# Kernel tuning notes

Hardware: AMD Instinct MI355X
Metric: run time of the kernel (lower is better)

The kernel has to match this reference:

```python
import jax, jax.numpy as jnp
from jax import lax
import numpy as np

V = 50000          # num_word; embedding table has V+1 rows
D = 512            # embedding_dim / d_model
H = 8              # nhead
FF = 2048          # dim_feedforward (hidden_dim)
L = 32             # num_label (incl START/STOP)
START, STOP = L - 2, L - 1
S = 2048           # sentence length
NEG = -10000.0


def setup_inputs() -> dict:
    k = jax.random.split(jax.random.key(0), 10)
    def rn(key, shape, s=0.02):
        return jax.random.normal(key, shape, jnp.float32) * s
    transitions = jax.random.normal(k[8], (L, L), jnp.float32)
    transitions = transitions.at[START, :].set(NEG).at[:, STOP].set(NEG)
    return {
        "sentence": jax.random.randint(k[0], (S,), 0, V + 1),
        "embed": rn(k[1], (V + 1, D), 1.0),
        "Wqkv": rn(k[2], (3 * D, D)), "bqkv": jnp.zeros((3 * D,), jnp.float32),
        "Wo": rn(k[3], (D, D)), "bo": jnp.zeros((D,), jnp.float32),
        "ln1_g": jnp.ones((D,), jnp.float32), "ln1_b": jnp.zeros((D,), jnp.float32),
        "W1": rn(k[4], (FF, D)), "b1": jnp.zeros((FF,), jnp.float32),
        "W2": rn(k[5], (D, FF)), "b2": jnp.zeros((D,), jnp.float32),
        "ln2_g": jnp.ones((D,), jnp.float32), "ln2_b": jnp.zeros((D,), jnp.float32),
        "Wt": rn(k[6], (L, D)), "bt": jnp.zeros((L,), jnp.float32),
        "transitions": transitions,
    }


def _ln(x, g, b):
    m = jnp.mean(x, -1, keepdims=True)
    v = jnp.var(x, -1, keepdims=True)
    return (x - m) * lax.rsqrt(v + 1e-5) * g + b


def _transformer_feats(sentence, embed, Wqkv, bqkv, Wo, bo, ln1_g, ln1_b,
                       W1, b1, W2, b2, ln2_g, ln2_b, Wt, bt):
    x = embed[sentence]                                   # [S, D]
    qkv = x @ Wqkv.T + bqkv                               # [S, 3D]
    q, k, v = jnp.split(qkv, 3, axis=-1)
    to_heads = lambda t: t.reshape(S, H, D // H).transpose(1, 0, 2)  # [H, S, dh]
    q, k, v = to_heads(q), to_heads(k), to_heads(v)
    att = jax.nn.softmax(jnp.einsum('hsd,htd->hst', q, k) / np.float32(np.sqrt(D // H)), axis=-1)
    o = jnp.einsum('hst,htd->hsd', att, v).transpose(1, 0, 2).reshape(S, D)
    # post-norm TransformerEncoderLayer (eval mode: dropout off), relu FFN
    x = _ln(x + o @ Wo.T + bo, ln1_g, ln1_b)
    ff = jax.nn.relu(x @ W1.T + b1) @ W2.T + b2
    x = _ln(x + ff, ln2_g, ln2_b)
    return x @ Wt.T + bt                                  # [S, L] emission scores


def _viterbi(feats, transitions):
    init = jnp.full((L,), NEG, jnp.float32).at[START].set(0.0)
    def step(prev, emit):
        scores = prev[None, :] + transitions              # [next_tag, prev_tag]
        bp = jnp.argmax(scores, axis=1)                   # best prev tag per next tag
        return jnp.max(scores, axis=1) + emit, bp
    last, bps = lax.scan(step, init, feats)               # bps: [S, L]
    terminal = last + transitions[STOP]
    best = jnp.argmax(terminal)
    def back(tag, bp):
        return bp[tag], tag
    _, path = lax.scan(back, best, bps, reverse=True)     # path[t] = best tag at step t
    return terminal[best], path


def reference(sentence, embed, Wqkv, bqkv, Wo, bo, ln1_g, ln1_b,
              W1, b1, W2, b2, ln2_g, ln2_b, Wt, bt, transitions):
    feats = _transformer_feats(sentence, embed, Wqkv, bqkv, Wo, bo, ln1_g, ln1_b,
                               W1, b1, W2, b2, ln2_g, ln2_b, Wt, bt)
    score, path = _viterbi(feats, transitions)
    return score, path
```

## Files before the change

### kernel.cpp

```cpp
#include <hip/hip_runtime.h>
#include <cstddef>

#define S_LEN 2048
#define D_MODEL 512
#define NHEAD 8
#define DH 64
#define FF_DIM 2048
#define L_TAGS 32
#define START_TAG 30
#define STOP_TAG 31
#define NEGV (-10000.0f)
#define QSCALE 0.18033688f

typedef unsigned int uint2v __attribute__((ext_vector_type(2)));
typedef __attribute__((ext_vector_type(8))) short short8v;
typedef __attribute__((ext_vector_type(4))) float f32x4;

union U8 { uint4 u; short8v s; };

__device__ __forceinline__ unsigned short f2bf(float f) {
  unsigned u = __float_as_uint(f);
  u += 0x7fff + ((u >> 16) & 1);
  return (unsigned short)(u >> 16);
}
__device__ __forceinline__ unsigned cvtpk(float lo, float hi) {
  unsigned r;
  asm("v_cvt_pk_bf16_f32 %0, %1, %2" : "=v"(r) : "v"(lo), "v"(hi));
  return r;
}

__global__ __launch_bounds__(256) void k_f2h4(const float* __restrict__ s0, short* __restrict__ d0,
                                              const float* __restrict__ s1, short* __restrict__ d1,
                                              const float* __restrict__ s2, short* __restrict__ d2,
                                              const float* __restrict__ s3, short* __restrict__ d3) {
  const int b = blockIdx.x;
  const float* src; short* dst; int i;
  if (b < 384)       { src = s0; dst = d0; i = b * 256 + threadIdx.x; }
  else if (b < 512)  { src = s1; dst = d1; i = (b - 384) * 256 + threadIdx.x; }
  else if (b < 1024) { src = s2; dst = d2; i = (b - 512) * 256 + threadIdx.x; }
  else               { src = s3; dst = d3; i = (b - 1024) * 256 + threadIdx.x; }
  f32x4 a = *(const f32x4*)(src + (size_t)i * 8);
  f32x4 c = *(const f32x4*)(src + (size_t)i * 8 + 4);
  U8 t;
  t.u.x = cvtpk(a[0], a[1]); t.u.y = cvtpk(a[2], a[3]);
  t.u.z = cvtpk(c[0], c[1]); t.u.w = cvtpk(c[2], c[3]);
  *(short8v*)(dst + (size_t)i * 8) = t.s;
}

__global__ __launch_bounds__(256, 2) void k_gemm_qkv(const int* __restrict__ sent,
                                                     const float* __restrict__ embed,
                                                     const short* __restrict__ B,
                                                     const float* __restrict__ bias,
                                                     short* __restrict__ C,
                                                     int N, int K) {
  __shared__ __align__(16) short As[2][128 * 64];
  __shared__ __align__(16) short Bs[2][128 * 64];
  const int tid = threadIdx.x;
  const int nwg = gridDim.x * gridDim.y;
  int lin = blockIdx.x + gridDim.x * blockIdx.y;
  int wk = (lin & 7) * (nwg >> 3) + (lin >> 3);
  const int bxs = wk % gridDim.x, bys = wk / gridDim.x;
  const int bm = bys * 128, bn = bxs * 128;
  const int w = tid >> 6, lane = tid & 63;
  const int wr = w >> 1, wc = w & 1;
  const int fr = lane & 15, kg = lane >> 4;
  const int srow = tid >> 1, sc0 = (tid & 1) * 4;
  const int swz = srow & 7;
  const float* gA = embed + (size_t)sent[bm + srow] * K + sc0 * 8;
  const short* gB = B + (size_t)(bn + srow) * K + sc0 * 8;
  f32x4 ra[8];
  short8v rb[4];
  f32x4 acc[4][4] = {};

  auto loadg = [&](int k0) {
#pragma unroll
    for (int c = 0; c < 4; ++c) {
      ra[2 * c] = *(const f32x4*)(gA + k0 + c * 8);
      ra[2 * c + 1] = *(const f32x4*)(gA + k0 + c * 8 + 4);
      rb[c] = *(const short8v*)(gB + k0 + c * 8);
    }
  };
  auto storeb = [&](int b) {
    short* dA = &As[b][srow * 64];
    short* dB = &Bs[b][srow * 64];
#pragma unroll
    for (int c = 0; c < 4; ++c) {
      U8 ta;
      ta.u.x = cvtpk(ra[2 * c][0], ra[2 * c][1]);
      ta.u.y = cvtpk(ra[2 * c][2], ra[2 * c][3]);
      ta.u.z = cvtpk(ra[2 * c + 1][0], ra[2 * c + 1][1]);
      ta.u.w = cvtpk(ra[2 * c + 1][2], ra[2 * c + 1][3]);
      *(short8v*)(dA + (((sc0 + c) ^ swz) << 3)) = ta.s;
      *(short8v*)(dB + (((sc0 + c) ^ swz) << 3)) = rb[c];
    }
  };

  loadg(0);
  storeb(0);
  __syncthreads();
  int cur = 0;
  const int fswz = fr & 7;
  for (int k0 = 0; k0 < K; k0 += 64) {
    const bool more = (k0 + 64) < K;
    if (more) loadg(k0 + 64);
    const short* rA = &As[cur][(wr * 64 + fr) * 64];
    const short* rB = &Bs[cur][(wc * 64 + fr) * 64];
#pragma unroll
    for (int ks = 0; ks < 2; ++ks) {
      const int co = ((ks * 4 + kg) ^ fswz) << 3;
      short8v af[4], bf[4];
#pragma unroll
      for (int rt = 0; rt < 4; ++rt) af[rt] = *(const short8v*)(rA + rt * 16 * 64 + co);
#pragma unroll
      for (int ct = 0; ct < 4; ++ct) bf[ct] = *(const short8v*)(rB + ct * 16 * 64 + co);
#pragma unroll
      for (int rt = 0; rt < 4; ++rt)
#pragma unroll
        for (int ct = 0; ct < 4; ++ct)
          acc[rt][ct] = __builtin_amdgcn_mfma_f32_16x16x32_bf16(af[rt], bf[ct], acc[rt][ct], 0, 0, 0);
    }
    if (more) storeb(cur ^ 1);
    __syncthreads();
    cur ^= 1;
  }
#pragma unroll
  for (int rt = 0; rt < 4; ++rt) {
#pragma unroll
    for (int ct = 0; ct < 4; ++ct) {
      f32x4 v = acc[rt][ct];
      const int row0 = bm + wr * 64 + rt * 16 + kg * 4;
      const int col = bn + wc * 64 + ct * 16 + fr;
      const float bs = bias[col];
#pragma unroll
      for (int j = 0; j < 4; ++j)
        C[(size_t)(row0 + j) * N + col] = (short)f2bf(v[j] + bs);
    }
  }
}

template <int RT, bool RELU, bool OBF>
__global__ __launch_bounds__(256, 2) void k_gemm_bf(const short* __restrict__ A,
                                                    const short* __restrict__ B,
                                                    const float* __restrict__ bias,
                                                    void* __restrict__ Cp,
                                                    int M, int N, int K) {
  constexpr int BM = RT * 32;
  constexpr int CH = (BM * 8) / 256;
  __shared__ __align__(16) short As[2][BM * 64];
  __shared__ __align__(16) short Bs[2][BM * 64];
  const int tid = threadIdx.x;
  const int nwg = gridDim.x * gridDim.y;
  int lin = blockIdx.x + gridDim.x * blockIdx.y;
  int wk = (lin & 7) * (nwg >> 3) + (lin >> 3);
  const int bxs = wk % gridDim.x, bys = wk / gridDim.x;
  const int bm = bys * BM, bn = bxs * BM;
  const int w = tid >> 6, lane = tid & 63;
  const int wr = w >> 1, wc = w & 1;
  const int fr = lane & 15, kg = lane >> 4;
  const int srow = (RT == 4) ? (tid >> 1) : (tid >> 2);
  const int sc0 = (RT == 4) ? ((tid & 1) * 4) : ((tid & 3) * 2);
  const int swz = srow & 7;
  const short* gA = A + (size_t)(bm + srow) * K + sc0 * 8;
  const short* gB = B + (size_t)(bn + srow) * K + sc0 * 8;
  short8v ra[CH], rb[CH];
  f32x4 acc[RT][RT] = {};

  auto loadg = [&](int k0) {
#pragma unroll
    for (int c = 0; c < CH; ++c) {
      ra[c] = *(const short8v*)(gA + k0 + c * 8);
      rb[c] = *(const short8v*)(gB + k0 + c * 8);
    }
  };
  auto storeb = [&](int b) {
    short* dA = &As[b][srow * 64];
    short* dB = &Bs[b][srow * 64];
#pragma unroll
    for (int c = 0; c < CH; ++c) {
      *(short8v*)(dA + (((sc0 + c) ^ swz) << 3)) = ra[c];
      *(short8v*)(dB + (((sc0 + c) ^ swz) << 3)) = rb[c];
    }
  };

  loadg(0);
  storeb(0);
  __syncthreads();
  int cur = 0;
  const int fswz = fr & 7;
  for (int k0 = 0; k0 < K; k0 += 64) {
    const bool more = (k0 + 64) < K;
    if (more) loadg(k0 + 64);
    const short* rA = &As[cur][(wr * (RT * 16) + fr) * 64];
    const short* rB = &Bs[cur][(wc * (RT * 16) + fr) * 64];
#pragma unroll
    for (int ks = 0; ks < 2; ++ks) {
      const int co = ((ks * 4 + kg) ^ fswz) << 3;
      short8v af[RT], bf[RT];
#pragma unroll
      for (int rt = 0; rt < RT; ++rt) af[rt] = *(const short8v*)(rA + rt * 16 * 64 + co);
#pragma unroll
      for (int ct = 0; ct < RT; ++ct) bf[ct] = *(const short8v*)(rB + ct * 16 * 64 + co);
#pragma unroll
      for (int rt = 0; rt < RT; ++rt)
#pragma unroll
        for (int ct = 0; ct < RT; ++ct)
          acc[rt][ct] = __builtin_amdgcn_mfma_f32_16x16x32_bf16(af[rt], bf[ct], acc[rt][ct], 0, 0, 0);
    }
    if (more) storeb(cur ^ 1);
    __syncthreads();
    cur ^= 1;
  }
#pragma unroll
  for (int rt = 0; rt < RT; ++rt) {
#pragma unroll
    for (int ct = 0; ct < RT; ++ct) {
      f32x4 v = acc[rt][ct];
      const int row0 = bm + wr * (RT * 16) + rt * 16 + kg * 4;
      const int col = bn + wc * (RT * 16) + ct * 16 + fr;
      const float bs = bias[col];
#pragma unroll
      for (int j = 0; j < 4; ++j) {
        float o = v[j] + bs;
        if (RELU) o = fmaxf(o, 0.f);
        if (OBF)
          ((short*)Cp)[(size_t)(row0 + j) * N + col] = (short)f2bf(o);
        else
          ((float*)Cp)[(size_t)(row0 + j) * N + col] = o;
      }
    }
  }
}

__global__ __launch_bounds__(256) void k_attn(const short* __restrict__ qkv,
                                              short* __restrict__ ob) {
  __shared__ __align__(16) short Ks[2][64 * 64];
  __shared__ __align__(16) short Vt[2][64 * 72];
  __shared__ __align__(16) short Pl[4][16 * 72];
  const int tid = threadIdx.x;
  const int b = blockIdx.x;
  const int h = b & 7;
  const int bq = (b >> 3) * 64;
  const int wq = tid >> 6, lane = tid & 63;
  const int fr = lane & 15, kg = lane >> 4;
  auto scale8 = [](short8v q) -> short8v {
    unsigned wv[4];
#pragma unroll
    for (int i = 0; i < 4; ++i) {
      float lo = __uint_as_float(((unsigned)(unsigned short)q[2 * i]) << 16) * QSCALE;
      float hi = __uint_as_float(((unsigned)(unsigned short)q[2 * i + 1]) << 16) * QSCALE;
      wv[i] = cvtpk(lo, hi);
    }
    U8 t;
    t.u.x = wv[0]; t.u.y = wv[1]; t.u.z = wv[2]; t.u.w = wv[3];
    return t.s;
  };
  short8v qf[2];
  {
    const short* qsrc = qkv + (size_t)(bq + wq * 16 + fr) * 1536 + h * DH;
    qf[0] = scale8(*(const short8v*)(qsrc + kg * 8));
    qf[1] = scale8(*(const short8v*)(qsrc + 32 + kg * 8));
  }
  float m[4], l[4];
  f32x4 oac[4] = {};
#pragma unroll
  for (int j = 0; j < 4; ++j) { m[j] = -1e30f; l[j] = 0.f; }

  const int srow = tid >> 2, sc0 = (tid & 3) * 2;
  const int kpair = tid & 31, dgrp = tid >> 5;
  short8v kr0, kr1, va, vb;
  auto loadt = [&](int kt) {
    const short* kbase = qkv + (size_t)(kt * 64 + srow) * 1536 + 512 + h * DH;
    kr0 = *(const short8v*)(kbase + sc0 * 8);
    kr1 = *(const short8v*)(kbase + sc0 * 8 + 8);
    const short* vbase = qkv + (size_t)(kt * 64 + 2 * kpair) * 1536 + 1024 + h * DH + dgrp * 8;
    va = *(const short8v*)(vbase);
    vb = *(const short8v*)(vbase + 1536);
  };
  auto storet = [&](int cu) {
    short* dk = &Ks[cu][srow * 64];
    *(short8v*)(dk + ((sc0 ^ (srow & 7)) << 3)) = kr0;
    *(short8v*)(dk + (((sc0 + 1) ^ (srow & 7)) << 3)) = kr1;
#pragma unroll
    for (int i = 0; i < 8; ++i) {
      unsigned u = ((unsigned)(unsigned short)va[i]) |
                   (((unsigned)(unsigned short)vb[i]) << 16);
      *(unsigned*)&Vt[cu][(dgrp * 8 + i) * 72 + 2 * kpair] = u;
    }
  };

  loadt(0);
  int cur = 0;
  for (int kt = 0; kt < 32; ++kt) {
    storet(cur);
    __syncthreads();
    if (kt < 31) loadt(kt + 1);
    f32x4 sac[4] = {};
#pragma unroll
    for (int ks = 0; ks < 2; ++ks) {
#pragma unroll
      for (int ct = 0; ct < 4; ++ct) {
        const int row = ct * 16 + fr;
        short8v bfr = *(const short8v*)&Ks[cur][row * 64 + (((ks * 4 + kg) ^ (row & 7)) << 3)];
        sac[ct] = __builtin_amdgcn_mfma_f32_16x16x32_bf16(qf[ks], bfr, sac[ct], 0, 0, 0);
      }
    }
    float pv[4][4];
#pragma unroll
    for (int j = 0; j < 4; ++j) {
      float v = fmaxf(fmaxf(sac[0][j], sac[1][j]), fmaxf(sac[2][j], sac[3][j]));
#pragma unroll
      for (int off = 1; off < 16; off <<= 1) v = fmaxf(v, __shfl_xor(v, off, 64));
      float mn = fmaxf(m[j], v);
      float f = __builtin_amdgcn_exp2f(m[j] - mn);
      m[j] = mn;
      float rs = 0.f;
#pragma unroll
      for (int ct = 0; ct < 4; ++ct) {
        pv[ct][j] = __builtin_amdgcn_exp2f(sac[ct][j] - mn);
        rs += pv[ct][j];
      }
#pragma unroll
      for (int off = 1; off < 16; off <<= 1) rs += __shfl_xor(rs, off, 64);
      l[j] = l[j] * f + rs;
#pragma unroll
      for (int ct = 0; ct < 4; ++ct) oac[ct][j] *= f;
    }
#pragma unroll
    for (int ct = 0; ct < 4; ++ct)
#pragma unroll
      for (int j = 0; j < 4; ++j)
        Pl[wq][(kg * 4 + j) * 72 + ct * 16 + fr] = (short)f2bf(pv[ct][j]);
#pragma unroll
    for (int ks = 0; ks < 2; ++ks) {
      short8v paf = *(const short8v*)&Pl[wq][fr * 72 + ks * 32 + kg * 8];
#pragma unroll
      for (int ct = 0; ct < 4; ++ct) {
        short8v vf = *(const short8v*)&Vt[cur][(ct * 16 + fr) * 72 + ks * 32 + kg * 8];
        oac[ct] = __builtin_amdgcn_mfma_f32_16x16x32_bf16(paf, vf, oac[ct], 0, 0, 0);
      }
    }
    cur ^= 1;
  }
#pragma unroll
  for (int j = 0; j < 4; ++j) {
    float inv = 1.f / l[j];
    const int q = bq + wq * 16 + kg * 4 + j;
#pragma unroll
    for (int ct = 0; ct < 4; ++ct)
      ob[(size_t)q * D_MODEL + h * DH + ct * 16 + fr] = (short)f2bf(oac[ct][j] * inv);
  }
}

__global__ __launch_bounds__(128) void k_ln(const float* __restrict__ a,
                                            const int* __restrict__ sent,
                                            const float* __restrict__ embed,
                                            const float* __restrict__ r,
                                            const float* __restrict__ g,
                                            const float* __restrict__ b,
                                            float* __restrict__ out,
                                            short* __restrict__ outh) {
  __shared__ float red[2];
  const int row = blockIdx.x, tid = threadIdx.x;
  const size_t off = (size_t)row * D_MODEL + tid * 4;
  float4 av;
  if (sent)
    av = *(const float4*)(embed + (size_t)sent[row] * D_MODEL + tid * 4);
  else
    av = *(const float4*)(a + off);
  float4 rv = *(const float4*)(r + off);
  float v0 = av.x + rv.x, v1 = av.y + rv.y, v2 = av.z + rv.z, v3 = av.w + rv.w;
  float s = v0 + v1 + v2 + v3;
#pragma unroll
  for (int d = 1; d < 64; d <<= 1) s += __shfl_xor(s, d, 64);
  if ((tid & 63) == 0) red[tid >> 6] = s;
  __syncthreads();
  float mean = (red[0] + red[1]) * (1.f / 512.f);
  __syncthreads();
  float d0 = v0 - mean, d1 = v1 - mean, d2 = v2 - mean, d3 = v3 - mean;
  float sq = d0 * d0 + d1 * d1 + d2 * d2 + d3 * d3;
#pragma unroll
  for (int d = 1; d < 64; d <<= 1) sq += __shfl_xor(sq, d, 64);
  if ((tid & 63) == 0) red[tid >> 6] = sq;
  __syncthreads();
  float inv = rsqrtf((red[0] + red[1]) * (1.f / 512.f) + 1e-5f);
  float4 gv = *(const float4*)(g + tid * 4);
  float4 bv = *(const float4*)(b + tid * 4);
  float4 o;
  o.x = d0 * inv * gv.x + bv.x;
  o.y = d1 * inv * gv.y + bv.y;
  o.z = d2 * inv * gv.z + bv.z;
  o.w = d3 * inv * gv.w + bv.w;
  *(float4*)(out + off) = o;
  if (outh) {
    uint2v t;
    t[0] = cvtpk(o.x, o.y);
    t[1] = cvtpk(o.z, o.w);
    *(uint2v*)(outh + off) = t;
  }
}

__global__ __launch_bounds__(128) void k_lnfeats(const float* __restrict__ a,
                                                 const float* __restrict__ r,
                                                 const float* __restrict__ g,
                                                 const float* __restrict__ b,
                                                 const float* __restrict__ Wt,
                                                 const float* __restrict__ bt,
                                                 float* __restrict__ feats) {
  __shared__ float red[2];
  __shared__ float part[2][32];
  const int row = blockIdx.x, tid = threadIdx.x;
  const size_t off = (size_t)row * D_MODEL + tid * 4;
  float4 av = *(const float4*)(a + off);
  float4 rv = *(const float4*)(r + off);
  float v0 = av.x + rv.x, v1 = av.y + rv.y, v2 = av.z + rv.z, v3 = av.w + rv.w;
  float s = v0 + v1 + v2 + v3;
#pragma unroll
  for (int d = 1; d < 64; d <<= 1) s += __shfl_xor(s, d, 64);
  if ((tid & 63) == 0) red[tid >> 6] = s;
  __syncthreads();
  float mean = (red[0] + red[1]) * (1.f / 512.f);
  __syncthreads();
  float d0 = v0 - mean, d1 = v1 - mean, d2 = v2 - mean, d3 = v3 - mean;
  float sq = d0 * d0 + d1 * d1 + d2 * d2 + d3 * d3;
#pragma unroll
  for (int d = 1; d < 64; d <<= 1) sq += __shfl_xor(sq, d, 64);
  if ((tid & 63) == 0) red[tid >> 6] = sq;
  __syncthreads();
  float inv = rsqrtf((red[0] + red[1]) * (1.f / 512.f) + 1e-5f);
  float4 gv = *(const float4*)(g + tid * 4);
  float4 bv = *(const float4*)(b + tid * 4);
  float4 o;
  o.x = d0 * inv * gv.x + bv.x;
  o.y = d1 * inv * gv.y + bv.y;
  o.z = d2 * inv * gv.z + bv.z;
  o.w = d3 * inv * gv.w + bv.w;
  const int lane = tid & 63, wv = tid >> 6;
#pragma unroll
  for (int l = 0; l < 32; ++l) {
    float4 wr4 = *(const float4*)(Wt + (size_t)l * D_MODEL + tid * 4);
    float p = o.x * wr4.x + o.y * wr4.y + o.z * wr4.z + o.w * wr4.w;
#pragma unroll
    for (int d = 1; d < 64; d <<= 1) p += __shfl_xor(p, d, 64);
    if (lane == 0) part[wv][l] = p;
  }
  __syncthreads();
  if (tid < 32) feats[(size_t)row * L_TAGS + tid] = part[0][tid] + part[1][tid] + bt[tid];
}

__global__ __launch_bounds__(64) void k_scan1(const float* __restrict__ feats,
                                              const float* __restrict__ T,
                                              float* __restrict__ P) {
  __shared__ float S[2][32];
  const int c = blockIdx.x >> 4;
  const int l = threadIdx.x;
  const int n = l & 31, pl = l >> 5;
  const int p = (blockIdx.x & 15) * 2 + pl;
  float Trow[32];
#pragma unroll
  for (int q = 0; q < 32; ++q) Trow[q] = T[n * 32 + q];
  const int tbase = c * 32;
  float er[4];
#pragma unroll
  for (int i = 0; i < 4; ++i) er[i] = feats[(tbase + i) * 32 + n];
  float a = T[n * 32 + p] + er[0];
  S[pl][n] = a;
  const float* fp = feats + (size_t)(tbase + 4) * 32 + n;
  er[0] = fp[0]; fp += 32;
  for (int u = 1; u < 32; ++u) {
    float e = er[u & 3];
    float enew = fp[0]; fp += 32;
    const float4* Sv = (const float4*)&S[pl][0];
    float g[32];
#pragma unroll
    for (int j4 = 0; j4 < 8; ++j4) {
      float4 sv = Sv[j4];
      g[j4 * 4 + 0] = sv.x + Trow[j4 * 4 + 0];
      g[j4 * 4 + 1] = sv.y + Trow[j4 * 4 + 1];
      g[j4 * 4 + 2] = sv.z + Trow[j4 * 4 + 2];
      g[j4 * 4 + 3] = sv.w + Trow[j4 * 4 + 3];
    }
#pragma unroll
    for (int st = 1; st < 32; st <<= 1)
#pragma unroll
      for (int j = 0; j < 32; j += 2 * st) g[j] = fmaxf(g[j], g[j + st]);
    a = g[0] + e;
    S[pl][n] = a;
    er[u & 3] = enew;
  }
  P[(size_t)c * 1024 + n * 32 + p] = a;
}

__global__ __launch_bounds__(64) void k_scan2(const float* __restrict__ P,
                                              const float* __restrict__ T,
                                              float* __restrict__ alphas,
                                              float* __restrict__ out,
                                              int* __restrict__ bestp) {
  __shared__ float Sa[32];
  const int l = threadIdx.x, n = l & 31, half = l >> 5;
  float a = (n == START_TAG) ? 0.f : NEGV;
  const float* pbase = P + n * 32 + half * 16;
  float4 pr[4];
#pragma unroll
  for (int j = 0; j < 4; ++j) pr[j] = *(const float4*)(pbase + j * 4);
  for (int c = 0; c < 64; ++c) {
    float4 nx[4];
#pragma unroll
    for (int j = 0; j < 4; ++j)
      nx[j] = *(const float4*)(pbase + (size_t)(c + 1) * 1024 + j * 4);
    alphas[(size_t)(c * 32) * 32 + n] = a;
    Sa[n] = a;
    const float4* Sv = (const float4*)&Sa[half * 16];
    float g[16];
#pragma unroll
    for (int j = 0; j < 4; ++j) {
      float4 sv = Sv[j];
      g[j * 4 + 0] = pr[j].x + sv.x;
      g[j * 4 + 1] = pr[j].y + sv.y;
      g[j * 4 + 2] = pr[j].z + sv.z;
      g[j * 4 + 3] = pr[j].w + sv.w;
    }
#pragma unroll
    for (int st = 1; st < 16; st <<= 1)
#pragma unroll
      for (int j = 0; j < 16; j += 2 * st) g[j] = fmaxf(g[j], g[j + st]);
    uint2v r = __builtin_amdgcn_permlane32_swap(__float_as_uint(g[0]),
                                                __float_as_uint(g[0]), false, false);
    a = fmaxf(__uint_as_float(r[0]), __uint_as_float(r[1]));
#pragma unroll
    for (int j = 0; j < 4; ++j) pr[j] = nx[j];
  }
  float term = a + T[STOP_TAG * 32 + n];
  float bv = term;
  int bi = n;
#pragma unroll
  for (int d = 1; d < 32; d <<= 1) {
    float ov = __shfl_xor(bv, d, 64);
    int oi = __shfl_xor(bi, d, 64);
    if (ov > bv || (ov == bv && oi < bi)) { bv = ov; bi = oi; }
  }
  if (l == 0) { out[0] = bv; *bestp = bi; }
}

__global__ __launch_bounds__(64) void k_scan3(const float* __restrict__ feats,
                                              const float* __restrict__ T,
                                              const float* __restrict__ alphas,
                                              unsigned char* __restrict__ cand,
                                              unsigned char* __restrict__ amap) {
  __shared__ float Sa[32];
  __shared__ unsigned char bpl[32][32];
  __shared__ unsigned cnd[256];
  const int c = blockIdx.x, l = threadIdx.x, n = l & 31, half = l >> 5;
  float Tr[16];
#pragma unroll
  for (int j = 0; j < 16; ++j) Tr[j] = T[n * 32 + half * 16 + j];
  const int tbase = c * 32;
  float a = alphas[(size_t)tbase * 32 + n];
  float er[4];
#pragma unroll
  for (int i = 0; i < 4; ++i) er[i] = feats[(tbase + i) * 32 + n];
  const float* fp = feats + (size_t)(tbase + 4) * 32 + n;
  Sa[n] = a;
  for (int u = 0; u < 32; ++u) {
    float e = er[u & 3];
    float enew = fp[0]; fp += 32;
    const float4* Sv = (const float4*)&Sa[half * 16];
    float4 s0 = Sv[0], s1 = Sv[1], s2 = Sv[2], s3 = Sv[3];
    float v[16] = {s0.x + Tr[0],  s0.y + Tr[1],  s0.z + Tr[2],  s0.w + Tr[3],
                   s1.x + Tr[4],  s1.y + Tr[5],  s1.z + Tr[6],  s1.w + Tr[7],
                   s2.x + Tr[8],  s2.y + Tr[9],  s2.z + Tr[10], s2.w + Tr[11],
                   s3.x + Tr[12], s3.y + Tr[13], s3.z + Tr[14], s3.w + Tr[15]};
    int id[16];
#pragma unroll
    for (int j = 0; j < 16; ++j) id[j] = half * 16 + j;
#pragma unroll
    for (int st = 1; st < 16; st <<= 1)
#pragma unroll
      for (int j = 0; j < 16; j += 2 * st)
        if (v[j + st] > v[j]) { v[j] = v[j + st]; id[j] = id[j + st]; }
    uint2v rv = __builtin_amdgcn_permlane32_swap(__float_as_uint(v[0]),
                                                 __float_as_uint(v[0]), false, false);
    uint2v ri = __builtin_amdgcn_permlane32_swap((unsigned)id[0], (unsigned)id[0],
                                                 false, false);
    float v0 = __uint_as_float(rv[0]), v1 = __uint_as_float(rv[1]);
    int i0 = (int)ri[0], i1 = (int)ri[1];
    float wvv = (v1 > v0) ? v1 : v0;
    int wi = (v1 > v0) ? i1 : i0;
    bpl[u][n] = (unsigned char)wi;
    a = wvv + e;
    Sa[n] = a;
    er[u & 3] = enew;
  }
  unsigned char* cnb = (unsigned char*)cnd;
  int tg = n;
  cnb[n * 32 + 31] = (unsigned char)n;
  for (int j = 31; j >= 1; --j) {
    tg = bpl[j][tg];
    cnb[n * 32 + (j - 1)] = (unsigned char)tg;
  }
  if (half == 0) amap[c * 32 + n] = bpl[0][tg];
#pragma unroll
  for (int i = 0; i < 4; ++i)
    ((unsigned*)(cand + (size_t)c * 1024))[l * 4 + i] = cnd[l * 4 + i];
}

__global__ __launch_bounds__(256) void k_trace2(const unsigned char* __restrict__ amap,
                                                const unsigned char* __restrict__ cand,
                                                const int* __restrict__ bestp,
                                                float* __restrict__ outp) {
  __shared__ unsigned char Am[64][32];
  __shared__ unsigned char et[64];
  const int tid = threadIdx.x;
  ((unsigned*)&Am[0][0])[tid] = ((const unsigned*)amap)[tid];
  ((unsigned*)&Am[32][0])[tid] = ((const unsigned*)amap)[tid + 256];
  __syncthreads();
  for (int d = 1; d < 64; d <<= 1) {
    unsigned char tmpv[8];
#pragma unroll
    for (int i = 0; i < 8; ++i) {
      int id = tid + 256 * i;
      int cc = id >> 5, e = id & 31;
      tmpv[i] = (cc + d < 64) ? Am[cc][Am[cc + d][e]] : Am[cc][e];
    }
    __syncthreads();
#pragma unroll
    for (int i = 0; i < 8; ++i) {
      int id = tid + 256 * i;
      Am[id >> 5][id & 31] = tmpv[i];
    }
    __syncthreads();
  }
  const int best = *bestp;
  if (tid < 64) et[tid] = (tid == 63) ? (unsigned char)best : Am[tid + 1][best];
  __syncthreads();
#pragma unroll
  for (int i = 0; i < 8; ++i) {
    int t = tid + 256 * i;
    int cc = t >> 5, j = t & 31;
    outp[1 + t] = (float)cand[(size_t)cc * 1024 + (size_t)et[cc] * 32 + j];
  }
}

extern "C" void kernel_launch(void* const* d_in, const int* in_sizes, int n_in,
                              void* d_out, int out_size, void* d_ws, size_t ws_size,
                              hipStream_t stream) {
  (void)in_sizes; (void)n_in; (void)out_size; (void)ws_size;
  const int* sent = (const int*)d_in[0];
  const float* embed = (const float*)d_in[1];
  const float* Wqkv = (const float*)d_in[2];
  const float* bqkv = (const float*)d_in[3];
  const float* Wo = (const float*)d_in[4];
  const float* bo = (const float*)d_in[5];
  const float* g1 = (const float*)d_in[6];
  const float* b1n = (const float*)d_in[7];
  const float* W1 = (const float*)d_in[8];
  const float* b1f = (const float*)d_in[9];
  const float* W2 = (const float*)d_in[10];
  const float* b2f = (const float*)d_in[11];
  const float* g2 = (const float*)d_in[12];
  const float* b2n = (const float*)d_in[13];
  const float* Wt = (const float*)d_in[14];
  const float* bt = (const float*)d_in[15];
  const float* T = (const float*)d_in[16];
  float* out = (float*)d_out;

  float* ws = (float*)d_ws;
  const size_t M1 = 1u << 20;
  short* qkvh = (short*)ws;
  short* obh = (short*)(ws + 2 * M1);
  float* yb = ws + 3 * M1;
  float* x1 = ws + 4 * M1;
  short* x1h = (short*)(ws + 5 * M1);
  short* ffbh = (short*)(ws + 6 * M1);
  float* zb = ws + 8 * M1;
  short* wqkvh = (short*)(ws + 10 * M1);
  short* woh = wqkvh + 786432;
  short* w1h = woh + 262144;
  short* w2h = w1h + 1048576;
  float* feats = ws + 11 * M1;
  float* alphas = feats + 2048 * 32 + 64;
  float* P = alphas + 2049 * 32 + 64;
  int* bestp = (int*)(P + 65 * 1024 + 64);
  unsigned char* cand = (unsigned char*)(bestp + 64);
  unsigned char* amap = cand + 2048 * 32;

  k_f2h4<<<dim3(1536), dim3(256), 0, stream>>>(Wqkv, wqkvh, Wo, woh, W1, w1h, W2, w2h);
  k_gemm_qkv<<<dim3(12, 16), dim3(256), 0, stream>>>(sent, embed, wqkvh, bqkv, qkvh, 1536, 512);
  k_attn<<<dim3(256), dim3(256), 0, stream>>>(qkvh, obh);
  k_gemm_bf<2, false, false><<<dim3(8, 32), dim3(256), 0, stream>>>(obh, woh, bo, yb, 2048, 512, 512);
  k_ln<<<dim3(2048), dim3(128), 0, stream>>>(nullptr, sent, embed, yb, g1, b1n, x1, x1h);
  k_gemm_bf<4, true, true><<<dim3(16, 16), dim3(256), 0, stream>>>(x1h, w1h, b1f, ffbh, 2048, 2048, 512);
  k_gemm_bf<2, false, false><<<dim3(8, 32), dim3(256), 0, stream>>>(ffbh, w2h, b2f, zb, 2048, 512, 2048);
  k_lnfeats<<<dim3(2048), dim3(128), 0, stream>>>(x1, zb, g2, b2n, Wt, bt, feats);
  k_scan1<<<dim3(1024), dim3(64), 0, stream>>>(feats, T, P);
  k_scan2<<<dim3(1), dim3(64), 0, stream>>>(P, T, alphas, out, bestp);
  k_scan3<<<dim3(64), dim3(64), 0, stream>>>(feats, T, alphas, cand, amap);
  k_trace2<<<dim3(1), dim3(256), 0, stream>>>(amap, cand, bestp, out);
}
```

Before: 179.1 us.

## Fuse Viterbi scan stages into one cooperative kernel with grid syncs

```diff
diff --git a/kernel.cpp b/kernel.cpp
--- a/kernel.cpp
+++ b/kernel.cpp
@@ -1,5 +1,8 @@
 #include <hip/hip_runtime.h>
+#include <hip/hip_cooperative_groups.h>
 #include <cstddef>
+
+namespace cg = cooperative_groups;
 
 #define S_LEN 2048
 #define D_MODEL 512
@@ -260,10 +263,10 @@
     qf[0] = scale8(*(const short8v*)(qsrc + kg * 8));
     qf[1] = scale8(*(const short8v*)(qsrc + 32 + kg * 8));
   }
-  float m[4], l[4];
+  float m[4], ls[4];
   f32x4 oac[4] = {};
 #pragma unroll
-  for (int j = 0; j < 4; ++j) { m[j] = -1e30f; l[j] = 0.f; }
+  for (int j = 0; j < 4; ++j) { m[j] = -1e30f; ls[j] = 0.f; }
 
   const int srow = tid >> 2, sc0 = (tid & 3) * 2;
   const int kpair = tid & 31, dgrp = tid >> 5;
@@ -319,9 +322,7 @@
         pv[ct][j] = __builtin_amdgcn_exp2f(sac[ct][j] - mn);
         rs += pv[ct][j];
       }
-#pragma unroll
-      for (int off = 1; off < 16; off <<= 1) rs += __shfl_xor(rs, off, 64);
-      l[j] = l[j] * f + rs;
+      ls[j] = ls[j] * f + rs;
 #pragma unroll
       for (int ct = 0; ct < 4; ++ct) oac[ct][j] *= f;
     }
@@ -343,7 +344,9 @@
   }
 #pragma unroll
   for (int j = 0; j < 4; ++j) {
-    float inv = 1.f / l[j];
+#pragma unroll
+    for (int off = 1; off < 16; off <<= 1) ls[j] += __shfl_xor(ls[j], off, 64);
+    float inv = 1.f / ls[j];
     const int q = bq + wq * 16 + kg * 4 + j;
 #pragma unroll
     for (int ct = 0; ct < 4; ++ct)
@@ -447,196 +450,196 @@
   if (tid < 32) feats[(size_t)row * L_TAGS + tid] = part[0][tid] + part[1][tid] + bt[tid];
 }
 
-__global__ __launch_bounds__(64) void k_scan1(const float* __restrict__ feats,
-                                              const float* __restrict__ T,
-                                              float* __restrict__ P) {
+__global__ __launch_bounds__(64) void k_viterbi(const float* __restrict__ feats,
+                                                const float* __restrict__ T,
+                                                float* __restrict__ P,
+                                                float* __restrict__ alphas,
+                                                float* __restrict__ out,
+                                                int* __restrict__ bestp,
+                                                unsigned char* __restrict__ cand,
+                                                unsigned char* __restrict__ amap) {
   __shared__ float S[2][32];
-  const int c = blockIdx.x >> 4;
-  const int l = threadIdx.x;
-  const int n = l & 31, pl = l >> 5;
-  const int p = (blockIdx.x & 15) * 2 + pl;
-  float Trow[32];
-#pragma unroll
-  for (int q = 0; q < 32; ++q) Trow[q] = T[n * 32 + q];
-  const int tbase = c * 32;
-  float er[4];
-#pragma unroll
-  for (int i = 0; i < 4; ++i) er[i] = feats[(tbase + i) * 32 + n];
-  float a = T[n * 32 + p] + er[0];
-  S[pl][n] = a;
-  const float* fp = feats + (size_t)(tbase + 4) * 32 + n;
-  er[0] = fp[0]; fp += 32;
-  for (int u = 1; u < 32; ++u) {
-    float e = er[u & 3];
-    float enew = fp[0]; fp += 32;
-    const float4* Sv = (const float4*)&S[pl][0];
-    float g[32];
-#pragma unroll
-    for (int j4 = 0; j4 < 8; ++j4) {
-      float4 sv = Sv[j4];
-      g[j4 * 4 + 0] = sv.x + Trow[j4 * 4 + 0];
-      g[j4 * 4 + 1] = sv.y + Trow[j4 * 4 + 1];
-      g[j4 * 4 + 2] = sv.z + Trow[j4 * 4 + 2];
-      g[j4 * 4 + 3] = sv.w + Trow[j4 * 4 + 3];
-    }
-#pragma unroll
-    for (int st = 1; st < 32; st <<= 1)
-#pragma unroll
-      for (int j = 0; j < 32; j += 2 * st) g[j] = fmaxf(g[j], g[j + st]);
-    a = g[0] + e;
-    S[pl][n] = a;
-    er[u & 3] = enew;
-  }
-  P[(size_t)c * 1024 + n * 32 + p] = a;
-}
-
-__global__ __launch_bounds__(64) void k_scan2(const float* __restrict__ P,
-                                              const float* __restrict__ T,
-                                              float* __restrict__ alphas,
-                                              float* __restrict__ out,
-                                              int* __restrict__ bestp) {
-  __shared__ float Sa[32];
-  const int l = threadIdx.x, n = l & 31, half = l >> 5;
-  float a = (n == START_TAG) ? 0.f : NEGV;
-  const float* pbase = P + n * 32 + half * 16;
-  float4 pr[4];
-#pragma unroll
-  for (int j = 0; j < 4; ++j) pr[j] = *(const float4*)(pbase + j * 4);
-  for (int c = 0; c < 64; ++c) {
-    float4 nx[4];
-#pragma unroll
-    for (int j = 0; j < 4; ++j)
-      nx[j] = *(const float4*)(pbase + (size_t)(c + 1) * 1024 + j * 4);
-    alphas[(size_t)(c * 32) * 32 + n] = a;
-    Sa[n] = a;
-    const float4* Sv = (const float4*)&Sa[half * 16];
-    float g[16];
-#pragma unroll
-    for (int j = 0; j < 4; ++j) {
-      float4 sv = Sv[j];
-      g[j * 4 + 0] = pr[j].x + sv.x;
-      g[j * 4 + 1] = pr[j].y + sv.y;
-      g[j * 4 + 2] = pr[j].z + sv.z;
-      g[j * 4 + 3] = pr[j].w + sv.w;
-    }
-#pragma unroll
-    for (int st = 1; st < 16; st <<= 1)
-#pragma unroll
-      for (int j = 0; j < 16; j += 2 * st) g[j] = fmaxf(g[j], g[j + st]);
-    uint2v r = __builtin_amdgcn_permlane32_swap(__float_as_uint(g[0]),
-                                                __float_as_uint(g[0]), false, false);
-    a = fmaxf(__uint_as_float(r[0]), __uint_as_float(r[1]));
-#pragma unroll
-    for (int j = 0; j < 4; ++j) pr[j] = nx[j];
-  }
-  float term = a + T[STOP_TAG * 32 + n];
-  float bv = term;
-  int bi = n;
-#pragma unroll
-  for (int d = 1; d < 32; d <<= 1) {
-    float ov = __shfl_xor(bv, d, 64);
-    int oi = __shfl_xor(bi, d, 64);
-    if (ov > bv || (ov == bv && oi < bi)) { bv = ov; bi = oi; }
-  }
-  if (l == 0) { out[0] = bv; *bestp = bi; }
-}
-
-__global__ __launch_bounds__(64) void k_scan3(const float* __restrict__ feats,
-                                              const float* __restrict__ T,
-                                              const float* __restrict__ alphas,
-                                              unsigned char* __restrict__ cand,
-                                              unsigned char* __restrict__ amap) {
   __shared__ float Sa[32];
   __shared__ unsigned char bpl[32][32];
   __shared__ unsigned cnd[256];
-  const int c = blockIdx.x, l = threadIdx.x, n = l & 31, half = l >> 5;
-  float Tr[16];
-#pragma unroll
-  for (int j = 0; j < 16; ++j) Tr[j] = T[n * 32 + half * 16 + j];
-  const int tbase = c * 32;
-  float a = alphas[(size_t)tbase * 32 + n];
-  float er[4];
-#pragma unroll
-  for (int i = 0; i < 4; ++i) er[i] = feats[(tbase + i) * 32 + n];
-  const float* fp = feats + (size_t)(tbase + 4) * 32 + n;
-  Sa[n] = a;
-  for (int u = 0; u < 32; ++u) {
-    float e = er[u & 3];
-    float enew = fp[0]; fp += 32;
-    const float4* Sv = (const float4*)&Sa[half * 16];
-    float4 s0 = Sv[0], s1 = Sv[1], s2 = Sv[2], s3 = Sv[3];
-    float v[16] = {s0.x + Tr[0],  s0.y + Tr[1],  s0.z + Tr[2],  s0.w + Tr[3],
-                   s1.x + Tr[4],  s1.y + Tr[5],  s1.z + Tr[6],  s1.w + Tr[7],
-                   s2.x + Tr[8],  s2.y + Tr[9],  s2.z + Tr[10], s2.w + Tr[11],
-                   s3.x + Tr[12], s3.y + Tr[13], s3.z + Tr[14], s3.w + Tr[15]};
-    int id[16];
-#pragma unroll
-    for (int j = 0; j < 16; ++j) id[j] = half * 16 + j;
-#pragma unroll
-    for (int st = 1; st < 16; st <<= 1)
-#pragma unroll
-      for (int j = 0; j < 16; j += 2 * st)
-        if (v[j + st] > v[j]) { v[j] = v[j + st]; id[j] = id[j + st]; }
-    uint2v rv = __builtin_amdgcn_permlane32_swap(__float_as_uint(v[0]),
-                                                 __float_as_uint(v[0]), false, false);
-    uint2v ri = __builtin_amdgcn_permlane32_swap((unsigned)id[0], (unsigned)id[0],
-                                                 false, false);
-    float v0 = __uint_as_float(rv[0]), v1 = __uint_as_float(rv[1]);
-    int i0 = (int)ri[0], i1 = (int)ri[1];
-    float wvv = (v1 > v0) ? v1 : v0;
-    int wi = (v1 > v0) ? i1 : i0;
-    bpl[u][n] = (unsigned char)wi;
-    a = wvv + e;
-    Sa[n] = a;
-    er[u & 3] = enew;
-  }
-  unsigned char* cnb = (unsigned char*)cnd;
-  int tg = n;
-  cnb[n * 32 + 31] = (unsigned char)n;
-  for (int j = 31; j >= 1; --j) {
-    tg = bpl[j][tg];
-    cnb[n * 32 + (j - 1)] = (unsigned char)tg;
-  }
-  if (half == 0) amap[c * 32 + n] = bpl[0][tg];
-#pragma unroll
-  for (int i = 0; i < 4; ++i)
-    ((unsigned*)(cand + (size_t)c * 1024))[l * 4 + i] = cnd[l * 4 + i];
-}
-
-__global__ __launch_bounds__(256) void k_trace2(const unsigned char* __restrict__ amap,
-                                                const unsigned char* __restrict__ cand,
-                                                const int* __restrict__ bestp,
-                                                float* __restrict__ outp) {
   __shared__ unsigned char Am[64][32];
   __shared__ unsigned char et[64];
-  const int tid = threadIdx.x;
-  ((unsigned*)&Am[0][0])[tid] = ((const unsigned*)amap)[tid];
-  ((unsigned*)&Am[32][0])[tid] = ((const unsigned*)amap)[tid + 256];
-  __syncthreads();
-  for (int d = 1; d < 64; d <<= 1) {
-    unsigned char tmpv[8];
-#pragma unroll
-    for (int i = 0; i < 8; ++i) {
-      int id = tid + 256 * i;
-      int cc = id >> 5, e = id & 31;
-      tmpv[i] = (cc + d < 64) ? Am[cc][Am[cc + d][e]] : Am[cc][e];
-    }
+  cg::grid_group grid = cg::this_grid();
+  const int blk = blockIdx.x;
+  const int l = threadIdx.x, n = l & 31, half = l >> 5;
+
+  {
+    const int c = blk >> 4;
+    const int pl = half;
+    const int p = (blk & 15) * 2 + pl;
+    float Trow[32];
+#pragma unroll
+    for (int q = 0; q < 32; ++q) Trow[q] = T[n * 32 + q];
+    const int tbase = c * 32;
+    float er[4];
+#pragma unroll
+    for (int i = 0; i < 4; ++i) er[i] = feats[(tbase + i) * 32 + n];
+    float a = T[n * 32 + p] + er[0];
+    S[pl][n] = a;
+    const float* fp = feats + (size_t)(tbase + 4) * 32 + n;
+    er[0] = fp[0]; fp += 32;
+    for (int u = 1; u < 32; ++u) {
+      float e = er[u & 3];
+      float enew = fp[0]; fp += 32;
+      const float4* Sv = (const float4*)&S[pl][0];
+      float g[32];
+#pragma unroll
+      for (int j4 = 0; j4 < 8; ++j4) {
+        float4 sv = Sv[j4];
+        g[j4 * 4 + 0] = sv.x + Trow[j4 * 4 + 0];
+        g[j4 * 4 + 1] = sv.y + Trow[j4 * 4 + 1];
+        g[j4 * 4 + 2] = sv.z + Trow[j4 * 4 + 2];
+        g[j4 * 4 + 3] = sv.w + Trow[j4 * 4 + 3];
+      }
+#pragma unroll
+      for (int st = 1; st < 32; st <<= 1)
+#pragma unroll
+        for (int j = 0; j < 32; j += 2 * st) g[j] = fmaxf(g[j], g[j + st]);
+      a = g[0] + e;
+      S[pl][n] = a;
+      er[u & 3] = enew;
+    }
+    P[(size_t)c * 1024 + n * 32 + p] = a;
+  }
+  grid.sync();
+
+  if (blk == 0) {
+    float a = (n == START_TAG) ? 0.f : NEGV;
+    const float* pbase = P + n * 32 + half * 16;
+    float4 pr[4];
+#pragma unroll
+    for (int j = 0; j < 4; ++j) pr[j] = *(const float4*)(pbase + j * 4);
+    for (int c = 0; c < 64; ++c) {
+      float4 nx[4];
+#pragma unroll
+      for (int j = 0; j < 4; ++j)
+        nx[j] = *(const float4*)(pbase + (size_t)(c + 1) * 1024 + j * 4);
+      alphas[(size_t)(c * 32) * 32 + n] = a;
+      Sa[n] = a;
+      const float4* Sv = (const float4*)&Sa[half * 16];
+      float g[16];
+#pragma unroll
+      for (int j = 0; j < 4; ++j) {
+        float4 sv = Sv[j];
+        g[j * 4 + 0] = pr[j].x + sv.x;
+        g[j * 4 + 1] = pr[j].y + sv.y;
+        g[j * 4 + 2] = pr[j].z + sv.z;
+        g[j * 4 + 3] = pr[j].w + sv.w;
+      }
+#pragma unroll
+      for (int st = 1; st < 16; st <<= 1)
+#pragma unroll
+        for (int j = 0; j < 16; j += 2 * st) g[j] = fmaxf(g[j], g[j + st]);
+      uint2v r = __builtin_amdgcn_permlane32_swap(__float_as_uint(g[0]),
+                                                  __float_as_uint(g[0]), false, false);
+      a = fmaxf(__uint_as_float(r[0]), __uint_as_float(r[1]));
+#pragma unroll
+      for (int j = 0; j < 4; ++j) pr[j] = nx[j];
+    }
+    float term = a + T[STOP_TAG * 32 + n];
+    float bv = term;
+    int bi = n;
+#pragma unroll
+    for (int d = 1; d < 32; d <<= 1) {
+      float ov = __shfl_xor(bv, d, 64);
+      int oi = __shfl_xor(bi, d, 64);
+      if (ov > bv || (ov == bv && oi < bi)) { bv = ov; bi = oi; }
+    }
+    if (l == 0) { out[0] = bv; *bestp = bi; }
+  }
+  grid.sync();
+
+  if (blk < 64) {
+    const int c = blk;
+    float Tr[16];
+#pragma unroll
+    for (int j = 0; j < 16; ++j) Tr[j] = T[n * 32 + half * 16 + j];
+    const int tbase = c * 32;
+    float a = alphas[(size_t)tbase * 32 + n];
+    float er[4];
+#pragma unroll
+    for (int i = 0; i < 4; ++i) er[i] = feats[(tbase + i) * 32 + n];
+    const float* fp = feats + (size_t)(tbase + 4) * 32 + n;
+    Sa[n] = a;
+    for (int u = 0; u < 32; ++u) {
+      float e = er[u & 3];
+      float enew = fp[0]; fp += 32;
+      const float4* Sv = (const float4*)&Sa[half * 16];
+      float4 s0 = Sv[0], s1 = Sv[1], s2 = Sv[2], s3 = Sv[3];
+      float v[16] = {s0.x + Tr[0],  s0.y + Tr[1],  s0.z + Tr[2],  s0.w + Tr[3],
+                     s1.x + Tr[4],  s1.y + Tr[5],  s1.z + Tr[6],  s1.w + Tr[7],
+                     s2.x + Tr[8],  s2.y + Tr[9],  s2.z + Tr[10], s2.w + Tr[11],
+                     s3.x + Tr[12], s3.y + Tr[13], s3.z + Tr[14], s3.w + Tr[15]};
+      int id[16];
+#pragma unroll
+      for (int j = 0; j < 16; ++j) id[j] = half * 16 + j;
+#pragma unroll
+      for (int st = 1; st < 16; st <<= 1)
+#pragma unroll
+        for (int j = 0; j < 16; j += 2 * st)
+          if (v[j + st] > v[j]) { v[j] = v[j + st]; id[j] = id[j + st]; }
+      uint2v rv = __builtin_amdgcn_permlane32_swap(__float_as_uint(v[0]),
+                                                   __float_as_uint(v[0]), false, false);
+      uint2v ri = __builtin_amdgcn_permlane32_swap((unsigned)id[0], (unsigned)id[0],
+                                                   false, false);
+      float v0 = __uint_as_float(rv[0]), v1 = __uint_as_float(rv[1]);
+      int i0 = (int)ri[0], i1 = (int)ri[1];
+      float wvv = (v1 > v0) ? v1 : v0;
+      int wi = (v1 > v0) ? i1 : i0;
+      bpl[u][n] = (unsigned char)wi;
+      a = wvv + e;
+      Sa[n] = a;
+      er[u & 3] = enew;
+    }
+    unsigned char* cnb = (unsigned char*)cnd;
+    int tg = n;
+    cnb[n * 32 + 31] = (unsigned char)n;
+    for (int j = 31; j >= 1; --j) {
+      tg = bpl[j][tg];
+      cnb[n * 32 + (j - 1)] = (unsigned char)tg;
+    }
+    if (half == 0) amap[c * 32 + n] = bpl[0][tg];
+#pragma unroll
+    for (int i = 0; i < 4; ++i)
+      ((unsigned*)(cand + (size_t)c * 1024))[l * 4 + i] = cnd[l * 4 + i];
+  }
+  grid.sync();
+
+  if (blk == 0) {
+#pragma unroll
+    for (int i = 0; i < 8; ++i)
+      ((unsigned*)&Am[0][0])[l + 64 * i] = ((const unsigned*)amap)[l + 64 * i];
     __syncthreads();
-#pragma unroll
-    for (int i = 0; i < 8; ++i) {
-      int id = tid + 256 * i;
-      Am[id >> 5][id & 31] = tmpv[i];
-    }
+    for (int d = 1; d < 64; d <<= 1) {
+      unsigned char tmpv[32];
+#pragma unroll
+      for (int i = 0; i < 32; ++i) {
+        int id = l + 64 * i;
+        int cc = id >> 5, e = id & 31;
+        tmpv[i] = (cc + d < 64) ? Am[cc][Am[cc + d][e]] : Am[cc][e];
+      }
+      __syncthreads();
+#pragma unroll
+      for (int i = 0; i < 32; ++i) {
+        int id = l + 64 * i;
+        Am[id >> 5][id & 31] = tmpv[i];
+      }
+      __syncthreads();
+    }
+    const int best = *bestp;
+    et[l] = (l == 63) ? (unsigned char)best : Am[l + 1][best];
     __syncthreads();
-  }
-  const int best = *bestp;
-  if (tid < 64) et[tid] = (tid == 63) ? (unsigned char)best : Am[tid + 1][best];
-  __syncthreads();
-#pragma unroll
-  for (int i = 0; i < 8; ++i) {
-    int t = tid + 256 * i;
-    int cc = t >> 5, j = t & 31;
-    outp[1 + t] = (float)cand[(size_t)cc * 1024 + (size_t)et[cc] * 32 + j];
+#pragma unroll
+    for (int i = 0; i < 32; ++i) {
+      int t = l + 64 * i;
+      int cc = t >> 5, j = t & 31;
+      out[1 + t] = (float)cand[(size_t)cc * 1024 + (size_t)et[cc] * 32 + j];
+    }
   }
 }
 
@@ -691,8 +694,9 @@
   k_gemm_bf<4, true, true><<<dim3(16, 16), dim3(256), 0, stream>>>(x1h, w1h, b1f, ffbh, 2048, 2048, 512);
   k_gemm_bf<2, false, false><<<dim3(8, 32), dim3(256), 0, stream>>>(ffbh, w2h, b2f, zb, 2048, 512, 2048);
   k_lnfeats<<<dim3(2048), dim3(128), 0, stream>>>(x1, zb, g2, b2n, Wt, bt, feats);
-  k_scan1<<<dim3(1024), dim3(64), 0, stream>>>(feats, T, P);
-  k_scan2<<<dim3(1), dim3(64), 0, stream>>>(P, T, alphas, out, bestp);
-  k_scan3<<<dim3(64), dim3(64), 0, stream>>>(feats, T, alphas, cand, amap);
-  k_trace2<<<dim3(1), dim3(256), 0, stream>>>(amap, cand, bestp, out);
-}
+  {
+    void* args[] = {(void*)&feats, (void*)&T, (void*)&P, (void*)&alphas,
+                    (void*)&out, (void*)&bestp, (void*)&cand, (void*)&amap};
+    hipLaunchCooperativeKernel((void*)k_viterbi, dim3(1024), dim3(64), args, 0, stream);
+  }
+}
```

New measurement: 474.9 us. 165% more time.
